# Optimization experiments

Hardware: AMD Instinct MI355X
Metric: run time of the kernel (lower is better)

The kernel has to match this reference:

```python
import jax, jax.numpy as jnp
import numpy as np
from math import ceil

B, T, FQ, D = 2, 48, 100, 512
H, DFF, L, WSZ = 8, 2048, 6, 8


def setup_inputs() -> dict:
    key = jax.random.key(0)
    ks = jax.random.split(key, 8)
    g = lambda k, shape: jax.random.normal(k, shape, jnp.float32) * 0.02
    return {
        "frame_queries": jax.random.normal(ks[0], (B, T, FQ, D), jnp.float32),
        "Wp": g(ks[1], (D, D)), "bp": jnp.zeros((D,), jnp.float32),
        "Wqkv": g(ks[2], (L, 3 * D, D)), "bqkv": jnp.zeros((L, 3 * D), jnp.float32),
        "Wo": g(ks[3], (L, D, D)), "bo": jnp.zeros((L, D), jnp.float32),
        "ln1_s": jnp.ones((L, D), jnp.float32), "ln1_b": jnp.zeros((L, D), jnp.float32),
        "W1": g(ks[4], (L, DFF, D)), "b1": jnp.zeros((L, DFF), jnp.float32),
        "W2": g(ks[5], (L, D, DFF)), "b2": jnp.zeros((L, D), jnp.float32),
        "ln2_s": jnp.ones((L, D), jnp.float32), "ln2_b": jnp.zeros((L, D), jnp.float32),
    }


def _ln(x, s, b, eps=1e-5):
    mu = x.mean(-1, keepdims=True)
    var = ((x - mu) ** 2).mean(-1, keepdims=True)
    return (x - mu) * jax.lax.rsqrt(var + eps) * s + b


def _mha(x, Wqkv_i, bqkv_i, Wo_i, bo_i, add_mask):
    # x: [Bw, S, C]; add_mask: None or [Bw, 1, S, S] additive float
    Bw, S, C = x.shape
    hd = C // H
    qkv = x @ Wqkv_i.T + bqkv_i
    q, k, v = jnp.split(qkv, 3, axis=-1)
    q = q.reshape(Bw, S, H, hd).transpose(0, 2, 1, 3)
    k = k.reshape(Bw, S, H, hd).transpose(0, 2, 1, 3)
    v = v.reshape(Bw, S, H, hd).transpose(0, 2, 1, 3)
    scores = jnp.einsum('bhqd,bhkd->bhqk', q, k) * jnp.float32(1.0 / np.sqrt(hd))
    if add_mask is not None:
        scores = scores + add_mask
    a = jax.nn.softmax(scores, axis=-1)
    o = jnp.einsum('bhqk,bhkd->bhqd', a, v).transpose(0, 2, 1, 3).reshape(Bw, S, C)
    return o @ Wo_i.T + bo_i


def _shift_mask():
    # padding mask is all-False (T % WSZ == 0), faithful construction of the
    # shifted-window additive mask as in the torch code.
    Nw = T // WSZ
    half = int(ceil(WSZ / 2))
    S = WSZ * FQ
    am = jnp.zeros((B, T), dtype=bool)
    r = jnp.roll(am, half, axis=1).reshape(B, Nw, WSZ)
    m = jnp.broadcast_to(r[..., None], (B, Nw, WSZ, WSZ))
    m = m.at[:, 0].set(m[:, 0] | m[:, 0].swapaxes(-1, -2))
    m = m.at[:, -1].set(m[:, -1] | m[:, -1].swapaxes(-1, -2))
    m = m.at[:, 0, :half, half:].set(True)
    m = m.at[:, 0, half:, :half].set(True)
    mfull = jnp.broadcast_to(m.reshape(B * Nw, WSZ, 1, WSZ, 1),
                             (B * Nw, WSZ, FQ, WSZ, FQ)).reshape(B * Nw, S, S)
    return (mfull.astype(jnp.float32) * -1000.0)[:, None]  # [B*Nw,1,S,S]


def reference(frame_queries, Wp, bp, Wqkv, bqkv, Wo, bo, ln1_s, ln1_b,
              W1, b1, W2, b2, ln2_s, ln2_b):
    Nw = T // WSZ
    half = int(ceil(WSZ / 2))
    S = WSZ * FQ
    x = frame_queries @ Wp.T + bp  # [B, T, FQ, D]
    shift_add = _shift_mask()
    for i in range(L):
        if i % 2 == 0:
            # plain window attention
            xw = x.reshape(B * Nw, S, D)
            xw = _ln(xw + _mha(xw, Wqkv[i], bqkv[i], Wo[i], bo[i], None),
                     ln1_s[i], ln1_b[i])
            x = xw.reshape(B, T, FQ, D)
        else:
            # shifted window attention
            xs = jnp.roll(x, half, axis=1)
            xw = xs.reshape(B * Nw, S, D)
            xw = _ln(xw + _mha(xw, Wqkv[i], bqkv[i], Wo[i], bo[i], shift_add),
                     ln1_s[i], ln1_b[i])
            x = jnp.roll(xw.reshape(B, T, FQ, D), -half, axis=1)
        # FFN (pointwise over channel dim)
        h = jax.nn.relu(x @ W1[i].T + b1[i]) @ W2[i].T + b2[i]
        x = _ln(x + h, ln2_s[i], ln2_b[i])
    return x  # [B, T, FQ, D] == 'lb t nq c'
```

## Files before the change

kernel.cpp:

```cpp
#include <hip/hip_runtime.h>


typedef float  f4    __attribute__((ext_vector_type(4)));
typedef __bf16 bf8   __attribute__((ext_vector_type(8)));
typedef unsigned short u16x8 __attribute__((ext_vector_type(8)));
typedef unsigned short u16x4 __attribute__((ext_vector_type(4)));

__device__ __forceinline__ unsigned short f2bf(float f) {
    unsigned int u = __builtin_bit_cast(unsigned int, f);
    u += 0x7fffu + ((u >> 16) & 1u);
    return (unsigned short)(u >> 16);
}
__device__ __forceinline__ float bf2f(unsigned short s) {
    return __builtin_bit_cast(float, ((unsigned int)s) << 16);
}

#define GLD16(gp, lp) __builtin_amdgcn_global_load_lds( \
    (const __attribute__((address_space(1))) void*)(gp), \
    (__attribute__((address_space(3))) void*)(lp), 16, 0, 0)

__device__ __forceinline__ int map_row(int r, int rshift) {
    if (!rshift) return r;
    int bb = r / 4800, rem = r % 4800;
    int tt = rem / 100, f = rem - tt * 100;
    return bb * 4800 + ((tt + rshift) % 48) * 100 + f;
}

template<int BM>
__global__ __launch_bounds__(256) void mfma_gemm(
    const unsigned short* __restrict__ A, const unsigned short* __restrict__ W,
    const float* __restrict__ bias, float* Cf, unsigned short* Cb,
    int M, int N, int K, int relu, int rshift, int qscale)
{
    constexpr int MI      = BM / 32;
    constexpr int ABUF    = BM * 32;
    constexpr int AROUNDS = BM / 64;
    __shared__ unsigned short As[2 * ABUF];
    __shared__ unsigned short Bs[2 * 4096];
    const int tid = threadIdx.x, lane = tid & 63, wave = tid >> 6;
    const int n0 = blockIdx.x * 128, m0 = blockIdx.y * BM;

    const unsigned short* ga[AROUNDS];
    unsigned short* la[AROUNDS];
    #pragma unroll
    for (int it = 0; it < AROUNDS; ++it) {
        int s = it * 256 + tid, row = s >> 2, cg = (s & 3) ^ ((row >> 1) & 3);
        ga[it] = A + (size_t)map_row(m0 + row, rshift) * K + cg * 8;
        la[it] = &As[(it * 256 + wave * 64) * 8];
    }
    const unsigned short* gb[2];
    unsigned short* lb[2];
    #pragma unroll
    for (int it = 0; it < 2; ++it) {
        int s = it * 256 + tid, row = s >> 2, cg = (s & 3) ^ ((row >> 1) & 3);
        gb[it] = W + (size_t)(n0 + row) * K + cg * 8;
        lb[it] = &Bs[(it * 256 + wave * 64) * 8];
    }

    const int wm = (wave >> 1) * (BM / 2), wn = (wave & 1) * 64;
    const int lr = lane & 15, quad = lane >> 4;

    f4 acc[MI][4];
    #pragma unroll
    for (int i = 0; i < MI; ++i)
        #pragma unroll
        for (int j = 0; j < 4; ++j) acc[i][j] = 0.f;

    #pragma unroll
    for (int it = 0; it < AROUNDS; ++it) GLD16(ga[it], la[it]);
    #pragma unroll
    for (int it = 0; it < 2; ++it) GLD16(gb[it], lb[it]);

    const int NK = K >> 5;
    for (int kt = 0; kt < NK; ++kt) {
        const int cb = kt & 1, nb = cb ^ 1;
        __syncthreads();
        if (kt + 1 < NK) {
            const int k1 = (kt + 1) << 5;
            #pragma unroll
            for (int it = 0; it < AROUNDS; ++it) GLD16(ga[it] + k1, la[it] + nb * ABUF);
            #pragma unroll
            for (int it = 0; it < 2; ++it)       GLD16(gb[it] + k1, lb[it] + nb * 4096);
        }
        const unsigned short* Ab = &As[cb * ABUF];
        const unsigned short* Bb = &Bs[cb * 4096];
        bf8 af[MI], bfr[4];
        #pragma unroll
        for (int mi = 0; mi < MI; ++mi) {
            int m = wm + mi * 16 + lr;
            int c = quad ^ ((m >> 1) & 3);
            af[mi] = __builtin_bit_cast(bf8, *(const u16x8*)&Ab[(m * 4 + c) * 8]);
        }
        #pragma unroll
        for (int ni = 0; ni < 4; ++ni) {
            int n = wn + ni * 16 + lr;
            int c = quad ^ ((n >> 1) & 3);
            bfr[ni] = __builtin_bit_cast(bf8, *(const u16x8*)&Bs[cb * 4096 + (n * 4 + c) * 8]);
        }
        #pragma unroll
        for (int mi = 0; mi < MI; ++mi)
            #pragma unroll
            for (int ni = 0; ni < 4; ++ni)
                acc[mi][ni] = __builtin_amdgcn_mfma_f32_16x16x32_bf16(
                    af[mi], bfr[ni], acc[mi][ni], 0, 0, 0);
        (void)Ab;
    }

    #pragma unroll
    for (int mi = 0; mi < MI; ++mi) {
        #pragma unroll
        for (int ni = 0; ni < 4; ++ni) {
            const int rowg = m0 + wm + mi * 16 + quad * 4;
            const int colg = n0 + wn + ni * 16 + lr;
            const float bv = bias[colg];
            const float sc = (qscale && colg < 512) ? 0.125f : 1.0f;
            #pragma unroll
            for (int r = 0; r < 4; ++r) {
                float v = (acc[mi][ni][r] + bv) * sc;
                if (relu) v = fmaxf(v, 0.f);
                const size_t off = (size_t)(rowg + r) * N + colg;
                if (Cf) Cf[off] = v;
                if (Cb) Cb[off] = f2bf(v);
            }
        }
    }
}

__global__ __launch_bounds__(320) void flash_attn_mfma(
    const unsigned short* __restrict__ qkv, unsigned short* __restrict__ o,
    int masked)
{
    __shared__ unsigned short Ks[2][2048];
    __shared__ unsigned short VT[2][64 * 34];
    __shared__ unsigned short Ps[5][576];

    const int bid = blockIdx.x;
    const int h = bid & 7, kk2 = bid >> 3;
    const int qt = kk2 % 10, w = kk2 / 10;
    const int tid = threadIdx.x, lane = tid & 63, wave = tid >> 6;
    const int lr = lane & 15, quad = lane >> 4;
    const int qb = qt * 80 + wave * 16;
    const size_t wbase = (size_t)w * 800 * 1536;
    const bool do_mask = masked && ((w % 6) == 0);

    bf8 aQ[2];
    {
        const unsigned short* qp =
            qkv + wbase + (size_t)(qb + lr) * 1536 + h * 64 + quad * 8;
        aQ[0] = __builtin_bit_cast(bf8, *(const u16x8*)qp);
        aQ[1] = __builtin_bit_cast(bf8, *(const u16x8*)(qp + 32));
    }

    const unsigned short* gk = qkv;
    int kw = 0;
    if (wave < 4) {
        int s = wave * 64 + lane, row = s >> 3, clog = (s & 7) ^ (row & 7);
        gk = qkv + wbase + (size_t)row * 1536 + 512 + h * 64 + clog * 8;
        kw = wave * 512;
    }
    const int vkey = tid >> 3, vd0 = (tid & 7) * 8;
    const unsigned short* gv =
        qkv + wbase + (size_t)vkey * 1536 + 1024 + h * 64 + vd0;

    float lsum = 0.f;
    f4 oacc[4];
    #pragma unroll
    for (int dt = 0; dt < 4; ++dt) oacc[dt] = 0.f;

    const bool qhl = (qb + lr) >= 400;

    if (wave < 4) GLD16(gk, &Ks[0][kw]);
    if (tid < 256) {
        u16x8 vv0 = *(const u16x8*)gv;
        #pragma unroll
        for (int j = 0; j < 8; ++j) VT[0][(vd0 + j) * 34 + vkey] = vv0[j];
    }

    for (int kt = 0; kt < 25; ++kt) {
        const int cb = kt & 1, nb = cb ^ 1;
        const int k0 = kt * 32;
        __syncthreads();

        u16x8 vv;
        const bool pf = (kt < 24);
        if (pf && wave < 4) GLD16(gk + (size_t)(k0 + 32) * 1536, &Ks[nb][kw]);
        if (pf && tid < 256) vv = *(const u16x8*)(gv + (size_t)(k0 + 32) * 1536);

        f4 st[2];
        st[0] = 0.f; st[1] = 0.f;
        #pragma unroll
        for (int kh = 0; kh < 2; ++kh) {
            const int cx = (kh * 4 + quad) ^ (lane & 7);
            bf8 kf0 = __builtin_bit_cast(bf8, *(const u16x8*)&Ks[cb][(lr * 8 + cx) * 8]);
            bf8 kf1 = __builtin_bit_cast(bf8, *(const u16x8*)&Ks[cb][((16 + lr) * 8 + cx) * 8]);
            st[0] = __builtin_amdgcn_mfma_f32_16x16x32_bf16(kf0, aQ[kh], st[0], 0, 0, 0);
            st[1] = __builtin_amdgcn_mfma_f32_16x16x32_bf16(kf1, aQ[kh], st[1], 0, 0, 0);
        }

        {
            u16x4 pk0, pk1;
            float ls = 0.f;
            #pragma unroll
            for (int r = 0; r < 4; ++r) {
                float a = st[0][r], b = st[1][r];
                if (do_mask) {
                    if (((k0 + quad * 4 + r) >= 400) != qhl)      a -= 1000.f;
                    if (((k0 + 16 + quad * 4 + r) >= 400) != qhl) b -= 1000.f;
                }
                float p0 = __expf(fminf(a, 80.f));
                float p1 = __expf(fminf(b, 80.f));
                ls += p0 + p1;
                pk0[r] = (unsigned short)(__builtin_bit_cast(unsigned int, p0) >> 16);
                pk1[r] = (unsigned short)(__builtin_bit_cast(unsigned int, p1) >> 16);
            }
            lsum += ls;
            *(u16x4*)&Ps[wave][lr * 36 + quad * 4]      = pk0;
            *(u16x4*)&Ps[wave][lr * 36 + 16 + quad * 4] = pk1;
        }

        if (pf && tid < 256) {
            #pragma unroll
            for (int j = 0; j < 8; ++j) VT[nb][(vd0 + j) * 34 + vkey] = vv[j];
        }

        bf8 aP = __builtin_bit_cast(bf8, *(const u16x8*)&Ps[wave][lr * 36 + quad * 8]);
        #pragma unroll
        for (int dt = 0; dt < 4; ++dt) {
            bf8 bV = __builtin_bit_cast(bf8,
                *(const u16x8*)&VT[cb][(dt * 16 + lr) * 34 + quad * 8]);
            oacc[dt] = __builtin_amdgcn_mfma_f32_16x16x32_bf16(aP, bV, oacc[dt], 0, 0, 0);
        }
    }

    {
        float l = lsum;
        l += __shfl_xor(l, 16);
        l += __shfl_xor(l, 32);
        float inv[4];
        #pragma unroll
        for (int r = 0; r < 4; ++r)
            inv[r] = 1.0f / __shfl(l, quad * 4 + r);
        #pragma unroll
        for (int dt = 0; dt < 4; ++dt)
            #pragma unroll
            for (int r = 0; r < 4; ++r)
                o[((size_t)w * 800 + qb + quad * 4 + r) * 512 + h * 64 + dt * 16 + lr] =
                    f2bf(oacc[dt][r] * inv[r]);
    }
}

__global__ __launch_bounds__(256) void add_ln_kernel(
    const unsigned short* xb, const unsigned short* dlt,
    const float* __restrict__ s, const float* __restrict__ b,
    float* outf, unsigned short* outb, int rshift)
{
    const int wave = threadIdx.x >> 6, lane = threadIdx.x & 63;
    const int row = blockIdx.x * 4 + wave;
    const int xrow = map_row(row, rshift);
    const int c = lane * 8;
    u16x8 xv = *(const u16x8*)(xb  + (size_t)xrow * 512 + c);
    u16x8 dv = *(const u16x8*)(dlt + (size_t)row  * 512 + c);
    f4 u0, u1;
    #pragma unroll
    for (int j = 0; j < 4; ++j) {
        u0[j] = bf2f(xv[j])     + bf2f(dv[j]);
        u1[j] = bf2f(xv[4 + j]) + bf2f(dv[4 + j]);
    }
    float sum = u0[0]+u0[1]+u0[2]+u0[3] + u1[0]+u1[1]+u1[2]+u1[3];
    #pragma unroll
    for (int o2 = 1; o2 < 64; o2 <<= 1) sum += __shfl_xor(sum, o2);
    const float mu = sum * (1.0f / 512.0f);
    f4 d0 = u0 - mu, d1 = u1 - mu;
    float sq = d0[0]*d0[0]+d0[1]*d0[1]+d0[2]*d0[2]+d0[3]*d0[3]
             + d1[0]*d1[0]+d1[1]*d1[1]+d1[2]*d1[2]+d1[3]*d1[3];
    #pragma unroll
    for (int o2 = 1; o2 < 64; o2 <<= 1) sq += __shfl_xor(sq, o2);
    const float rs = rsqrtf(sq * (1.0f / 512.0f) + 1e-5f);
    f4 s0 = *(const f4*)(s + c), s1 = *(const f4*)(s + c + 4);
    f4 b0 = *(const f4*)(b + c), b1 = *(const f4*)(b + c + 4);
    f4 y0, y1;
    #pragma unroll
    for (int j = 0; j < 4; ++j) { y0[j] = d0[j]*rs*s0[j]+b0[j]; y1[j] = d1[j]*rs*s1[j]+b1[j]; }
    u16x8 ob;
    #pragma unroll
    for (int j = 0; j < 4; ++j) { ob[j] = f2bf(y0[j]); ob[4+j] = f2bf(y1[j]); }
    *(u16x8*)(outb + (size_t)xrow * 512 + c) = ob;
    if (outf) {
        float* of = outf + (size_t)xrow * 512 + c;
        *(f4*)of = y0; *(f4*)(of + 4) = y1;
    }
}

__global__ __launch_bounds__(256) void cast_f2b_kernel(
    const float* __restrict__ in, unsigned short* __restrict__ out, int n4)
{
    const int i = blockIdx.x * 256 + threadIdx.x;
    if (i >= n4) return;
    f4 v = ((const f4*)in)[i];
    u16x4 o4 = {f2bf(v[0]), f2bf(v[1]), f2bf(v[2]), f2bf(v[3])};
    ((u16x4*)out)[i] = o4;
}

extern "C" void kernel_launch(void* const* d_in, const int* in_sizes, int n_in,
                              void* d_out, int out_size, void* d_ws, size_t ws_size,
                              hipStream_t stream)
{
    const float* fq   = (const float*)d_in[0];
    const float* Wp   = (const float*)d_in[1];
    const float* bp   = (const float*)d_in[2];
    const float* Wqkv = (const float*)d_in[3];
    const float* bqkv = (const float*)d_in[4];
    const float* Wo   = (const float*)d_in[5];
    const float* bo   = (const float*)d_in[6];
    const float* l1s  = (const float*)d_in[7];
    const float* l1b  = (const float*)d_in[8];
    const float* W1   = (const float*)d_in[9];
    const float* b1   = (const float*)d_in[10];
    const float* W2   = (const float*)d_in[11];
    const float* b2   = (const float*)d_in[12];
    const float* l2s  = (const float*)d_in[13];
    const float* l2b  = (const float*)d_in[14];
    float* out = (float*)d_out;

    unsigned short* xb   = (unsigned short*)d_ws;
    unsigned short* qkvb = xb + 4915200;
    unsigned short* hbuf = qkvb + 14745600;
    unsigned short* wbuf = hbuf + 19660800;
    unsigned short* obuf = hbuf;
    unsigned short* t1b  = qkvb;
    unsigned short* fqb  = hbuf;
    unsigned short* wqA = wbuf;
    unsigned short* woA = wqA + 4718592;
    unsigned short* w1A = woA + 1572864;
    unsigned short* w2A = w1A + 6291456;
    unsigned short* wpA = w2A + 6291456;

    const dim3 blk(256);
    cast_f2b_kernel<<<dim3(4800), blk, 0, stream>>>(fq,   fqb, 1228800);
    cast_f2b_kernel<<<dim3(4608), blk, 0, stream>>>(Wqkv, wqA, 1179648);
    cast_f2b_kernel<<<dim3(1536), blk, 0, stream>>>(Wo,   woA, 393216);
    cast_f2b_kernel<<<dim3(6144), blk, 0, stream>>>(W1,   w1A, 1572864);
    cast_f2b_kernel<<<dim3(6144), blk, 0, stream>>>(W2,   w2A, 1572864);
    cast_f2b_kernel<<<dim3(256),  blk, 0, stream>>>(Wp,   wpA, 65536);
    mfma_gemm<64><<<dim3(4, 150), blk, 0, stream>>>(fqb, wpA, bp, nullptr, xb,
                                                    9600, 512, 512, 0, 0, 0);

    for (int i = 0; i < 6; ++i) {
        const int rsh = (i & 1) ? 44 : 0;
        const unsigned short* wq = wqA + (size_t)i * 786432;
        const unsigned short* wo = woA + (size_t)i * 262144;
        const unsigned short* w1 = w1A + (size_t)i * 1048576;
        const unsigned short* w2 = w2A + (size_t)i * 1048576;
        mfma_gemm<128><<<dim3(12, 75), blk, 0, stream>>>(xb, wq, bqkv + i * 1536,
                                                         nullptr, qkvb, 9600, 1536, 512, 0, rsh, 1);
        flash_attn_mfma<<<dim3(960), dim3(320), 0, stream>>>(qkvb, obuf, i & 1);
        mfma_gemm<64><<<dim3(4, 150), blk, 0, stream>>>(obuf, wo, bo + i * 512,
                                                        nullptr, t1b, 9600, 512, 512, 0, 0, 0);
        add_ln_kernel<<<dim3(2400), blk, 0, stream>>>(xb, t1b, l1s + i * 512, l1b + i * 512,
                                                      nullptr, xb, rsh);
        mfma_gemm<128><<<dim3(16, 75), blk, 0, stream>>>(xb, w1, b1 + i * 2048,
                                                         nullptr, hbuf, 9600, 2048, 512, 1, 0, 0);
        mfma_gemm<64><<<dim3(4, 150), blk, 0, stream>>>(hbuf, w2, b2 + i * 512,
                                                        nullptr, t1b, 9600, 512, 2048, 0, 0, 0);
        add_ln_kernel<<<dim3(2400), blk, 0, stream>>>(xb, t1b, l2s + i * 512, l2b + i * 512,
                                                      (i == 5) ? out : nullptr, xb, 0);
    }
}
```

Measured before the change: 1.248 ms.

## Triple-buffer GEMM LDS staging with explicit vmcnt waits for two-deep prefetch

The bf16 MFMA GEMM moves from two separate double-buffered A/B LDS arrays to a single three-slot ring buffer. Two K-tiles are kept in flight via global_load_lds. Explicit s_waitcnt vmcnt counts replace the generic __syncthreads, so each iteration waits only for the current tile and leaves the next one outstanding. The aim is to hide more global-memory latency behind the MFMAs, at the cost of more LDS per block, which may lower occupancy.

```diff
diff --git a/kernel.cpp b/kernel.cpp
--- a/kernel.cpp
+++ b/kernel.cpp
@@ -34,56 +34,65 @@
 {
     constexpr int MI      = BM / 32;
     constexpr int ABUF    = BM * 32;
+    constexpr int SB      = ABUF + 4096;
     constexpr int AROUNDS = BM / 64;
-    __shared__ unsigned short As[2 * ABUF];
-    __shared__ unsigned short Bs[2 * 4096];
+    constexpr int LPT     = AROUNDS + 2;
+    __shared__ unsigned short Ls[3 * SB];
     const int tid = threadIdx.x, lane = tid & 63, wave = tid >> 6;
     const int n0 = blockIdx.x * 128, m0 = blockIdx.y * BM;
 
     const unsigned short* ga[AROUNDS];
-    unsigned short* la[AROUNDS];
     #pragma unroll
     for (int it = 0; it < AROUNDS; ++it) {
         int s = it * 256 + tid, row = s >> 2, cg = (s & 3) ^ ((row >> 1) & 3);
         ga[it] = A + (size_t)map_row(m0 + row, rshift) * K + cg * 8;
-        la[it] = &As[(it * 256 + wave * 64) * 8];
     }
     const unsigned short* gb[2];
-    unsigned short* lb[2];
     #pragma unroll
     for (int it = 0; it < 2; ++it) {
         int s = it * 256 + tid, row = s >> 2, cg = (s & 3) ^ ((row >> 1) & 3);
         gb[it] = W + (size_t)(n0 + row) * K + cg * 8;
-        lb[it] = &Bs[(it * 256 + wave * 64) * 8];
     }
 
     const int wm = (wave >> 1) * (BM / 2), wn = (wave & 1) * 64;
     const int lr = lane & 15, quad = lane >> 4;
 
+    auto STAGE = [&](int kt2, int buf) {
+        const int k1 = kt2 << 5;
+        unsigned short* Lb = &Ls[buf * SB];
+        #pragma unroll
+        for (int it = 0; it < AROUNDS; ++it)
+            GLD16(ga[it] + k1, &Lb[(it * 256 + wave * 64) * 8]);
+        #pragma unroll
+        for (int it = 0; it < 2; ++it)
+            GLD16(gb[it] + k1, &Lb[ABUF + (it * 256 + wave * 64) * 8]);
+    };
+
     f4 acc[MI][4];
     #pragma unroll
     for (int i = 0; i < MI; ++i)
         #pragma unroll
         for (int j = 0; j < 4; ++j) acc[i][j] = 0.f;
 
-    #pragma unroll
-    for (int it = 0; it < AROUNDS; ++it) GLD16(ga[it], la[it]);
-    #pragma unroll
-    for (int it = 0; it < 2; ++it) GLD16(gb[it], lb[it]);
-
     const int NK = K >> 5;
+    STAGE(0, 0);
+    STAGE(1, 1);
+
+    int cb = 0;
     for (int kt = 0; kt < NK; ++kt) {
-        const int cb = kt & 1, nb = cb ^ 1;
-        __syncthreads();
         if (kt + 1 < NK) {
-            const int k1 = (kt + 1) << 5;
-            #pragma unroll
-            for (int it = 0; it < AROUNDS; ++it) GLD16(ga[it] + k1, la[it] + nb * ABUF);
-            #pragma unroll
-            for (int it = 0; it < 2; ++it)       GLD16(gb[it] + k1, lb[it] + nb * 4096);
-        }
-        const unsigned short* Ab = &As[cb * ABUF];
-        const unsigned short* Bb = &Bs[cb * 4096];
+            if constexpr (BM == 128) asm volatile("s_waitcnt vmcnt(4)" ::: "memory");
+            else                     asm volatile("s_waitcnt vmcnt(3)" ::: "memory");
+        } else {
+            asm volatile("s_waitcnt vmcnt(0)" ::: "memory");
+        }
+        __builtin_amdgcn_s_barrier();
+        __builtin_amdgcn_sched_barrier(0);
+        const int ib = (cb == 0) ? 2 : cb - 1;
+        if (kt + 2 < NK) STAGE(kt + 2, ib);
+
+        const unsigned short* Ab = &Ls[cb * SB];
+        const unsigned short* Bb = &Ls[cb * SB + ABUF];
         bf8 af[MI], bfr[4];
         #pragma unroll
         for (int mi = 0; mi < MI; ++mi) {
@@ -95,7 +104,7 @@
         for (int ni = 0; ni < 4; ++ni) {
             int n = wn + ni * 16 + lr;
             int c = quad ^ ((n >> 1) & 3);
-            bfr[ni] = __builtin_bit_cast(bf8, *(const u16x8*)&Bs[cb * 4096 + (n * 4 + c) * 8]);
+            bfr[ni] = __builtin_bit_cast(bf8, *(const u16x8*)&Bb[(n * 4 + c) * 8]);
         }
         #pragma unroll
         for (int mi = 0; mi < MI; ++mi)
@@ -103,7 +112,8 @@
             for (int ni = 0; ni < 4; ++ni)
                 acc[mi][ni] = __builtin_amdgcn_mfma_f32_16x16x32_bf16(
                     af[mi], bfr[ni], acc[mi][ni], 0, 0, 0);
-        (void)Ab;
+        __builtin_amdgcn_sched_barrier(0);
+        cb = (cb + 1 == 3) ? 0 : cb + 1;
     }
 
     #pragma unroll
```

New measurement: 1.219 ms. 1.02x faster.
